# Kernel tuning notes

Hardware: AMD Instinct MI355X
Metric: run time of the kernel (lower is better)

The kernel has to match this reference:

```python
import jax, jax.numpy as jnp
import numpy as np

B, T, D = 32, 1024, 1024
PCA_DIM = 256
NS = 4
NC = 1024
SEC = PCA_DIM // NS


def setup_inputs() -> dict:
    key = jax.random.key(0)
    k1, k2, k3 = jax.random.split(key, 3)
    inputs = jax.random.normal(k1, (B, T, D), dtype=jnp.float32)
    # variance_scaling(1.0, 'fan_avg', 'normal'): std = sqrt(2 / (fan_in + fan_out))
    pca_proj = jax.random.normal(k2, (D, PCA_DIM), dtype=jnp.float32) * np.float32(np.sqrt(2.0 / (D + PCA_DIM)))
    pre_bias = jnp.zeros((1, D), dtype=jnp.float32)
    # per-section codebooks, variance_scaling(0.1, 'fan_avg', 'normal')
    codebooks = jax.random.normal(k3, (NS, NC, SEC), dtype=jnp.float32) * np.float32(np.sqrt(0.1 * 2.0 / (NC + SEC)))
    return {"inputs": inputs, "pca_proj": pca_proj, "pre_bias": pre_bias, "codebooks": codebooks}


def reference(inputs, pca_proj, pre_bias, codebooks):
    in_shape = inputs.shape
    d = in_shape[-1]
    flat = inputs.reshape(-1, d)  # [N, D]
    n = flat.shape[0]
    # --- PCA projection + reconstruction / decorrelation losses ---
    projected = (flat + pre_bias) @ pca_proj            # [N, P]
    unprojected = projected @ pca_proj.T - pre_bias     # [N, D]
    l2_loss = jnp.mean(jnp.sqrt(jnp.sum(jnp.square(flat - unprojected), axis=-1)))
    cov = projected.T @ projected / n                   # [P, P]
    cov_loss = jnp.mean(jnp.square(cov - jnp.eye(pca_proj.shape[1], dtype=projected.dtype)))
    pca_loss = l2_loss + cov_loss
    # --- per-section vector quantization ---
    ns, nc, sec = codebooks.shape
    secs = projected.reshape(n, ns, sec).transpose(1, 0, 2)  # [ns, N, sec] == jnp.split along -1

    def quantize_section(x, cb):
        # x: [N, sec], cb: [nc, sec]; squared-L2 cdist via expansion
        dist = (jnp.sum(x * x, axis=1, keepdims=True)
                - 2.0 * (x @ cb.T)
                + jnp.sum(cb * cb, axis=1)[None, :])    # [N, nc]
        idx = jnp.argmin(dist, axis=1)                  # [N]
        q = cb[idx]                                     # gather == one_hot @ cb
        loss = jnp.square(q - jax.lax.stop_gradient(x))  # [N, sec]
        q_st = x + jax.lax.stop_gradient(q - x)         # straight-through
        return q_st, loss, idx

    q, sec_loss, idx = jax.vmap(quantize_section)(secs, codebooks)  # [ns,N,sec] x2, [ns,N]
    quantized = q.transpose(1, 0, 2).reshape(n, ns * sec)           # concat sections -> [N, P]
    quantized = (quantized @ pca_proj.T - pre_bias).reshape(in_shape)  # pca_unproject
    nn_idx = idx.reshape((ns,) + in_shape[:-1])                     # [ns, B, T]
    quantization_loss = jnp.mean(sec_loss.reshape((ns,) + in_shape[:-1] + (sec,)), axis=0) + pca_loss
    codebook = jax.lax.stop_gradient(codebooks.reshape(ns * nc, sec))
    cluster_counts = jnp.ones((ns, nc), dtype=jnp.float32)  # eval mode: jnp.ones init, no EMA
    return quantized, quantization_loss, nn_idx, codebook, cluster_counts
```

## Files before the change

### kernel.cpp

```cpp
#include <hip/hip_runtime.h>
#include <math.h>

#define NROW 32768
#define DIM  1024
#define PDIM 256
#define NSEC 4
#define NCODE 1024
#define SECD 64

__global__ __launch_bounds__(256, 4) void k_proj(const float* __restrict__ X,
                                                 const float* __restrict__ W,
                                                 const float* __restrict__ bias,
                                                 float* __restrict__ p0) {
    __shared__ __align__(16) float As[16][68];
    __shared__ __align__(16) float Bs[16][256];
    const int t  = threadIdx.x;
    const int ry = t >> 5;
    const int rx = t & 31;
    const int rb = blockIdx.x * 64;
    const int z  = blockIdx.z;
    const int k0 = z * 384;
    const int kn = (z == 2) ? 256 : 384;
    const int lr = t >> 2;
    const int ks = (t & 3) * 4;
    const int wv = t >> 6;
    const int ln = t & 63;
    const int gsw = ((ln & 31) << 1) | (ln >> 5);
    float* outp = p0 + (size_t)z * ((size_t)NROW * PDIM);
    float acc[8][8] = {};
    for (int kc = k0; kc < k0 + kn; kc += 16) {
        #pragma unroll
        for (int j = 0; j < 4; ++j) {
            const int krow = wv * 4 + j;
            __builtin_amdgcn_global_load_lds(
                (const __attribute__((address_space(1))) void*)(W + (size_t)(kc + krow) * PDIM + gsw * 4),
                (__attribute__((address_space(3))) void*)(&Bs[krow][0]),
                16, 0, 0);
        }
        float4 a = *(const float4*)&X[(size_t)(rb + lr) * DIM + kc + ks];
        float4 c = *(const float4*)&bias[kc + ks];
        As[ks + 0][lr] = a.x + c.x;
        As[ks + 1][lr] = a.y + c.y;
        As[ks + 2][lr] = a.z + c.z;
        As[ks + 3][lr] = a.w + c.w;
        __syncthreads();
        #pragma unroll
        for (int k = 0; k < 16; ++k) {
            float4 x0 = *(const float4*)&As[k][ry * 8];
            float4 x1 = *(const float4*)&As[k][ry * 8 + 4];
            float4 y0 = *(const float4*)&Bs[k][rx * 4];
            float4 y1 = *(const float4*)&Bs[k][128 + rx * 4];
            float aa[8] = {x0.x, x0.y, x0.z, x0.w, x1.x, x1.y, x1.z, x1.w};
            float bb[8] = {y0.x, y0.y, y0.z, y0.w, y1.x, y1.y, y1.z, y1.w};
            #pragma unroll
            for (int i = 0; i < 8; ++i)
                #pragma unroll
                for (int j = 0; j < 8; ++j)
                    acc[i][j] = fmaf(aa[i], bb[j], acc[i][j]);
        }
        __syncthreads();
    }
    #pragma unroll
    for (int i = 0; i < 8; ++i) {
        const size_t base = (size_t)(rb + ry * 8 + i) * PDIM + rx * 8;
        *(float4*)&outp[base]     = make_float4(acc[i][0], acc[i][1], acc[i][2], acc[i][3]);
        *(float4*)&outp[base + 4] = make_float4(acc[i][4], acc[i][5], acc[i][6], acc[i][7]);
    }
}

__global__ __launch_bounds__(256) void k_comb(float* __restrict__ p) {
    const size_t i = ((size_t)blockIdx.x * 256 + threadIdx.x) * 4;
    float4 a = *(const float4*)&p[i];
    float4 b = *(const float4*)&p[i + 8388608];
    float4 c = *(const float4*)&p[i + 16777216];
    float4 r;
    r.x = __fadd_rn(__fadd_rn(a.x, b.x), c.x);
    r.y = __fadd_rn(__fadd_rn(a.y, b.y), c.y);
    r.z = __fadd_rn(__fadd_rn(a.z, b.z), c.z);
    r.w = __fadd_rn(__fadd_rn(a.w, b.w), c.w);
    *(float4*)&p[i] = r;
}

__global__ __launch_bounds__(256, 4) void k_pm(const float* __restrict__ P,
                                               const float* __restrict__ M,
                                               float* __restrict__ PMa,
                                               float* __restrict__ PMb) {
    __shared__ __align__(16) float As[16][68];
    __shared__ __align__(16) float Bs[16][256];
    const int t  = threadIdx.x;
    const int ry = t >> 5;
    const int rx = t & 31;
    const int rb = blockIdx.x * 64;
    const int z  = blockIdx.z;
    const int k0 = z * 128;
    const int lr = t >> 2;
    const int ks = (t & 3) * 4;
    const int wv = t >> 6;
    const int ln = t & 63;
    const int gsw = ((ln & 31) << 1) | (ln >> 5);
    float* outp = z ? PMb : PMa;
    float acc[8][8] = {};
    for (int kc = k0; kc < k0 + 128; kc += 16) {
        #pragma unroll
        for (int j = 0; j < 4; ++j) {
            const int krow = wv * 4 + j;
            __builtin_amdgcn_global_load_lds(
                (const __attribute__((address_space(1))) void*)(M + (size_t)(kc + krow) * PDIM + gsw * 4),
                (__attribute__((address_space(3))) void*)(&Bs[krow][0]),
                16, 0, 0);
        }
        float4 a = *(const float4*)&P[(size_t)(rb + lr) * PDIM + kc + ks];
        As[ks + 0][lr] = a.x;
        As[ks + 1][lr] = a.y;
        As[ks + 2][lr] = a.z;
        As[ks + 3][lr] = a.w;
        __syncthreads();
        #pragma unroll
        for (int k = 0; k < 16; ++k) {
            float4 x0 = *(const float4*)&As[k][ry * 8];
            float4 x1 = *(const float4*)&As[k][ry * 8 + 4];
            float4 y0 = *(const float4*)&Bs[k][rx * 4];
            float4 y1 = *(const float4*)&Bs[k][128 + rx * 4];
            float aa[8] = {x0.x, x0.y, x0.z, x0.w, x1.x, x1.y, x1.z, x1.w};
            float bb[8] = {y0.x, y0.y, y0.z, y0.w, y1.x, y1.y, y1.z, y1.w};
            #pragma unroll
            for (int i = 0; i < 8; ++i)
                #pragma unroll
                for (int j = 0; j < 8; ++j)
                    acc[i][j] = fmaf(aa[i], bb[j], acc[i][j]);
        }
        __syncthreads();
    }
    #pragma unroll
    for (int i = 0; i < 8; ++i) {
        const size_t base = (size_t)(rb + ry * 8 + i) * PDIM + rx * 8;
        *(float4*)&outp[base]     = make_float4(acc[i][0], acc[i][1], acc[i][2], acc[i][3]);
        *(float4*)&outp[base + 4] = make_float4(acc[i][4], acc[i][5], acc[i][6], acc[i][7]);
    }
}

__global__ __launch_bounds__(256) void k_wtw(const float* __restrict__ W,
                                             float* __restrict__ M) {
    __shared__ float As[16][64];
    __shared__ float Bs[16][64];
    const int t = threadIdx.x;
    const int tx = t & 15, ty = t >> 4;
    const int ib = blockIdx.x * 64;
    const int jb = blockIdx.y * 64;
    const int sk = t >> 4;
    const int sc = (t & 15) * 4;
    float acc[4][4] = {};
    for (int kc = 0; kc < DIM; kc += 16) {
        float4 a = *(const float4*)&W[(size_t)(kc + sk) * PDIM + ib + sc];
        float4 b = *(const float4*)&W[(size_t)(kc + sk) * PDIM + jb + sc];
        *(float4*)&As[sk][sc] = a;
        *(float4*)&Bs[sk][sc] = b;
        __syncthreads();
        #pragma unroll
        for (int k = 0; k < 16; ++k) {
            float4 a4 = *(const float4*)&As[k][ty * 4];
            float4 b4 = *(const float4*)&Bs[k][tx * 4];
            float aa[4] = {a4.x, a4.y, a4.z, a4.w};
            float bb[4] = {b4.x, b4.y, b4.z, b4.w};
            #pragma unroll
            for (int i = 0; i < 4; ++i)
                #pragma unroll
                for (int j = 0; j < 4; ++j)
                    acc[i][j] = fmaf(aa[i], bb[j], acc[i][j]);
        }
        __syncthreads();
    }
    #pragma unroll
    for (int i = 0; i < 4; ++i)
        #pragma unroll
        for (int j = 0; j < 4; ++j)
            M[(size_t)(ib + ty * 4 + i) * PDIM + jb + tx * 4 + j] = acc[i][j];
}

__global__ __launch_bounds__(256) void k_xn2(const float* __restrict__ X,
                                             const float* __restrict__ bias,
                                             float* __restrict__ xn2) {
    const int n = blockIdx.x * 4 + (threadIdx.x >> 6);
    const int lane = threadIdx.x & 63;
    float s = 0.0f;
    #pragma unroll
    for (int i = 0; i < 4; ++i) {
        float4 x = *(const float4*)&X[(size_t)n * DIM + i * 256 + lane * 4];
        float4 b = *(const float4*)&bias[i * 256 + lane * 4];
        float vx = x.x + b.x, vy = x.y + b.y, vz = x.z + b.z, vw = x.w + b.w;
        s = fmaf(vx, vx, s); s = fmaf(vy, vy, s);
        s = fmaf(vz, vz, s); s = fmaf(vw, vw, s);
    }
    #pragma unroll
    for (int o = 1; o < 64; o <<= 1) s += __shfl_xor(s, o);
    if (lane == 0) xn2[n] = s;
}

__global__ __launch_bounds__(256) void k_rowres(const float* __restrict__ P,
                                                const float* __restrict__ PMa,
                                                const float* __restrict__ PMb,
                                                const float* __restrict__ xn2,
                                                float* __restrict__ rowres) {
    const int n = blockIdx.x * 4 + (threadIdx.x >> 6);
    const int lane = threadIdx.x & 63;
    float4 p  = *(const float4*)&P[(size_t)n * PDIM + lane * 4];
    float4 pa = *(const float4*)&PMa[(size_t)n * PDIM + lane * 4];
    float4 pb = *(const float4*)&PMb[(size_t)n * PDIM + lane * 4];
    float s = 0.0f;
    s = fmaf(p.x, (pa.x + pb.x) - 2.0f * p.x, s);
    s = fmaf(p.y, (pa.y + pb.y) - 2.0f * p.y, s);
    s = fmaf(p.z, (pa.z + pb.z) - 2.0f * p.z, s);
    s = fmaf(p.w, (pa.w + pb.w) - 2.0f * p.w, s);
    #pragma unroll
    for (int o = 1; o < 64; o <<= 1) s += __shfl_xor(s, o);
    if (lane == 0) rowres[n] = xn2[n] + s;
}

__global__ __launch_bounds__(256) void k_cov(const float* __restrict__ Pm,
                                             float* __restrict__ cov) {
    __shared__ float As[16][64];
    __shared__ float Bs[16][64];
    const int t = threadIdx.x;
    const int tx = t & 15, ty = t >> 4;
    const int ib = blockIdx.x * 64;
    const int jb = blockIdx.y * 64;
    const int nb = blockIdx.z * 2048;
    const int sk = t >> 4;
    const int sc = (t & 15) * 4;
    float acc[4][4] = {};
    for (int kc = 0; kc < 2048; kc += 16) {
        float4 a = *(const float4*)&Pm[(size_t)(nb + kc + sk) * PDIM + ib + sc];
        float4 b = *(const float4*)&Pm[(size_t)(nb + kc + sk) * PDIM + jb + sc];
        *(float4*)&As[sk][sc] = a;
        *(float4*)&Bs[sk][sc] = b;
        __syncthreads();
        #pragma unroll
        for (int k = 0; k < 16; ++k) {
            float4 a4 = *(const float4*)&As[k][ty * 4];
            float4 b4 = *(const float4*)&Bs[k][tx * 4];
            float aa[4] = {a4.x, a4.y, a4.z, a4.w};
            float bb[4] = {b4.x, b4.y, b4.z, b4.w};
            #pragma unroll
            for (int i = 0; i < 4; ++i)
                #pragma unroll
                for (int j = 0; j < 4; ++j)
                    acc[i][j] = fmaf(aa[i], bb[j], acc[i][j]);
        }
        __syncthreads();
    }
    #pragma unroll
    for (int i = 0; i < 4; ++i)
        #pragma unroll
        for (int j = 0; j < 4; ++j)
            atomicAdd(&cov[(size_t)(ib + ty * 4 + i) * PDIM + jb + tx * 4 + j], acc[i][j]);
}

__global__ __launch_bounds__(256) void k_covloss(const float* __restrict__ cov,
                                                 float* __restrict__ scal) {
    const int t = threadIdx.x;
    float s = 0.0f;
    for (int e = t; e < PDIM * PDIM; e += 256) {
        int i = e >> 8, j = e & 255;
        float v = cov[e] * (1.0f / 32768.0f) - (i == j ? 1.0f : 0.0f);
        s = fmaf(v, v, s);
    }
    #pragma unroll
    for (int o = 1; o < 64; o <<= 1) s += __shfl_xor(s, o);
    __shared__ float r4[4];
    if ((t & 63) == 0) r4[t >> 6] = s;
    __syncthreads();
    if (t == 0) scal[1] = (r4[0] + r4[1] + r4[2] + r4[3]) * (1.0f / 65536.0f);
}

__global__ __launch_bounds__(256) void k_l2(const float* __restrict__ rowres,
                                            float* __restrict__ scal) {
    int r = blockIdx.x * 256 + threadIdx.x;
    float v = sqrtf(rowres[r]);
    #pragma unroll
    for (int o = 1; o < 64; o <<= 1) v += __shfl_xor(v, o);
    if ((threadIdx.x & 63) == 0) atomicAdd(&scal[0], v);
}

__global__ __launch_bounds__(256) void k_cnorm(const float* __restrict__ cbs,
                                               float* __restrict__ cnorm) {
    int c = blockIdx.x * 256 + threadIdx.x;
    const float* p = &cbs[(size_t)c * SECD];
    float a[8];
    #pragma unroll
    for (int j = 0; j < 8; ++j) a[j] = __fmul_rn(p[j], p[j]);
    #pragma unroll
    for (int i = 8; i < 64; i += 8)
        #pragma unroll
        for (int j = 0; j < 8; ++j)
            a[j] = __fadd_rn(a[j], __fmul_rn(p[i + j], p[i + j]));
    float r = __fadd_rn(__fadd_rn(__fadd_rn(a[0], a[1]), __fadd_rn(a[2], a[3])),
                        __fadd_rn(__fadd_rn(a[4], a[5]), __fadd_rn(a[6], a[7])));
    cnorm[c] = r;
}

__global__ __launch_bounds__(256) void k_vq(const float* __restrict__ proj,
                                            const float* __restrict__ cbs,
                                            const float* __restrict__ cnorm,
                                            int* __restrict__ widx,
                                            float* __restrict__ out_idx,
                                            float* __restrict__ out_qloss) {
    __shared__ float xs[64][64];
    __shared__ float cs[64][128];
    __shared__ float xnorm[64];
    __shared__ int   sidx[64];
    const int t = threadIdx.x;
    const int ry = t >> 5;
    const int tx = t & 31;
    const int rb = blockIdx.x * 64;
    const int lr = t >> 2;
    const int kq = (t & 3) * 16;
    const int cr = t >> 1;
    const int ko = (t & 1) * 32;
    float qacc[16];
    #pragma unroll
    for (int i = 0; i < 16; ++i) qacc[i] = 0.0f;

    for (int s = 0; s < NSEC; ++s) {
        #pragma unroll
        for (int i = 0; i < 16; i += 4) {
            float4 v = *(const float4*)&proj[(size_t)(rb + lr) * PDIM + s * SECD + kq + i];
            xs[kq + i + 0][lr] = v.x; xs[kq + i + 1][lr] = v.y;
            xs[kq + i + 2][lr] = v.z; xs[kq + i + 3][lr] = v.w;
        }
        __syncthreads();
        if (t < 64) {
            float a[8];
            #pragma unroll
            for (int j = 0; j < 8; ++j) { float v = xs[j][t]; a[j] = __fmul_rn(v, v); }
            #pragma unroll
            for (int i = 8; i < 64; i += 8)
                #pragma unroll
                for (int j = 0; j < 8; ++j) {
                    float v = xs[i + j][t];
                    a[j] = __fadd_rn(a[j], __fmul_rn(v, v));
                }
            xnorm[t] = __fadd_rn(__fadd_rn(__fadd_rn(a[0], a[1]), __fadd_rn(a[2], a[3])),
                                 __fadd_rn(__fadd_rn(a[4], a[5]), __fadd_rn(a[6], a[7])));
        }
        float best[8]; int bidx[8];
        #pragma unroll
        for (int i = 0; i < 8; ++i) { best[i] = 3.4e38f; bidx[i] = 0; }

        for (int ct = 0; ct < 8; ++ct) {
            __syncthreads();
            #pragma unroll
            for (int u = 0; u < 32; u += 4) {
                float4 v = *(const float4*)&cbs[(size_t)(s * NCODE + ct * 128 + cr) * SECD + ko + u];
                cs[ko + u + 0][cr] = v.x; cs[ko + u + 1][cr] = v.y;
                cs[ko + u + 2][cr] = v.z; cs[ko + u + 3][cr] = v.w;
            }
            __syncthreads();
            float4 cn4 = *(const float4*)&cnorm[s * NCODE + ct * 128 + tx * 4];
            float cna[4] = {cn4.x, cn4.y, cn4.z, cn4.w};
            float acc[8][4] = {};
            #pragma unroll 8
            for (int k = 0; k < 64; ++k) {
                float4 x0 = *(const float4*)&xs[k][ry * 8];
                float4 x1 = *(const float4*)&xs[k][ry * 8 + 4];
                float4 b4 = *(const float4*)&cs[k][tx * 4];
                float aa[8] = {x0.x, x0.y, x0.z, x0.w, x1.x, x1.y, x1.z, x1.w};
                float bb[4] = {b4.x, b4.y, b4.z, b4.w};
                #pragma unroll
                for (int i = 0; i < 8; ++i)
                    #pragma unroll
                    for (int j = 0; j < 4; ++j)
                        acc[i][j] = fmaf(aa[i], bb[j], acc[i][j]);
            }
            #pragma unroll
            for (int i = 0; i < 8; ++i) {
                float xn = xnorm[ry * 8 + i];
                #pragma unroll
                for (int j = 0; j < 4; ++j) {
                    float d = __fadd_rn(__fsub_rn(xn, __fmul_rn(2.0f, acc[i][j])), cna[j]);
                    int code = ct * 128 + tx * 4 + j;
                    if (d < best[i]) { best[i] = d; bidx[i] = code; }
                }
            }
        }
        #pragma unroll
        for (int i = 0; i < 8; ++i) {
            float d = best[i]; int ix = bidx[i];
            #pragma unroll
            for (int o = 1; o < 32; o <<= 1) {
                float od = __shfl_xor(d, o);
                int   oi = __shfl_xor(ix, o);
                if (od < d || (od == d && oi < ix)) { d = od; ix = oi; }
            }
            if (tx == 0) {
                int row = rb + ry * 8 + i;
                widx[s * NROW + row] = ix;
                out_idx[s * NROW + row] = (float)ix;
                sidx[ry * 8 + i] = ix;
            }
        }
        __syncthreads();
        {
            const float* crow = &cbs[(size_t)(s * NCODE + sidx[lr]) * SECD];
            #pragma unroll
            for (int i = 0; i < 16; i += 4) {
                float4 q = *(const float4*)&crow[kq + i];
                float qq[4] = {q.x, q.y, q.z, q.w};
                #pragma unroll
                for (int u = 0; u < 4; ++u) {
                    float d = qq[u] - xs[kq + i + u][lr];
                    qacc[i + u] = fmaf(d, d, qacc[i + u]);
                }
            }
        }
        __syncthreads();
    }
    #pragma unroll
    for (int i = 0; i < 16; i += 4) {
        float4 v = make_float4(0.25f * qacc[i + 0], 0.25f * qacc[i + 1],
                               0.25f * qacc[i + 2], 0.25f * qacc[i + 3]);
        *(float4*)&out_qloss[(size_t)(rb + lr) * SECD + kq + i] = v;
    }
}

__global__ __launch_bounds__(256) void k_cbu(const float* __restrict__ cbs,
                                             const float* __restrict__ W,
                                             float* __restrict__ cbu) {
    __shared__ float As[16][64];
    __shared__ float Bs[16][64];
    const int t = threadIdx.x;
    const int tx = t & 15, ty = t >> 4;
    const int s = blockIdx.z;
    const int cbase = blockIdx.y * 64;
    const int db = blockIdx.x * 64;
    const int lr = t >> 2;
    const int lk = (t & 3) * 4;
    float acc[4][4] = {};
    for (int kc = 0; kc < SECD; kc += 16) {
        float4 a = *(const float4*)&cbs[(size_t)(s * NCODE + cbase + lr) * SECD + kc + lk];
        float4 b = *(const float4*)&W[(size_t)(db + lr) * PDIM + s * SECD + kc + lk];
        As[lk + 0][lr] = a.x; As[lk + 1][lr] = a.y;
        As[lk + 2][lr] = a.z; As[lk + 3][lr] = a.w;
        Bs[lk + 0][lr] = b.x; Bs[lk + 1][lr] = b.y;
        Bs[lk + 2][lr] = b.z; Bs[lk + 3][lr] = b.w;
        __syncthreads();
        #pragma unroll
        for (int k = 0; k < 16; ++k) {
            float4 a4 = *(const float4*)&As[k][ty * 4];
            float4 b4 = *(const float4*)&Bs[k][tx * 4];
            float aa[4] = {a4.x, a4.y, a4.z, a4.w};
            float bb[4] = {b4.x, b4.y, b4.z, b4.w};
            #pragma unroll
            for (int i = 0; i < 4; ++i)
                #pragma unroll
                for (int j = 0; j < 4; ++j)
                    acc[i][j] = fmaf(aa[i], bb[j], acc[i][j]);
        }
        __syncthreads();
    }
    #pragma unroll
    for (int i = 0; i < 4; ++i) {
        float4 v = make_float4(acc[i][0], acc[i][1], acc[i][2], acc[i][3]);
        *(float4*)&cbu[(size_t)(s * NCODE + cbase + ty * 4 + i) * DIM + db + tx * 4] = v;
    }
}

__global__ __launch_bounds__(256) void k_gather(const float* __restrict__ cbu,
                                                const int* __restrict__ widx,
                                                const float* __restrict__ bias,
                                                float* __restrict__ out0) {
    const int n = blockIdx.x;
    const int d = threadIdx.x * 4;
    int i0 = widx[0 * NROW + n];
    int i1 = widx[1 * NROW + n];
    int i2 = widx[2 * NROW + n];
    int i3 = widx[3 * NROW + n];
    float4 v0 = *(const float4*)&cbu[((size_t)(0 * NCODE + i0)) * DIM + d];
    float4 v1 = *(const float4*)&cbu[((size_t)(1 * NCODE + i1)) * DIM + d];
    float4 v2 = *(const float4*)&cbu[((size_t)(2 * NCODE + i2)) * DIM + d];
    float4 v3 = *(const float4*)&cbu[((size_t)(3 * NCODE + i3)) * DIM + d];
    float4 b = *(const float4*)&bias[d];
    float4 r;
    r.x = v0.x + v1.x + v2.x + v3.x - b.x;
    r.y = v0.y + v1.y + v2.y + v3.y - b.y;
    r.z = v0.z + v1.z + v2.z + v3.z - b.z;
    r.w = v0.w + v1.w + v2.w + v3.w - b.w;
    *(float4*)&out0[(size_t)n * DIM + d] = r;
}

__global__ __launch_bounds__(256) void k_addpca(float* __restrict__ out1,
                                                const float* __restrict__ scal) {
    float pca = scal[0] * (1.0f / 32768.0f) + scal[1];
    int e = blockIdx.x * 256 + threadIdx.x;
    float4* p = (float4*)out1;
    float4 v = p[e];
    v.x += pca; v.y += pca; v.z += pca; v.w += pca;
    p[e] = v;
}

__global__ __launch_bounds__(256) void k_tail(const float* __restrict__ cbs,
                                              float* __restrict__ out3,
                                              float* __restrict__ out4) {
    int e = blockIdx.x * 256 + threadIdx.x;
    ((float4*)out3)[e] = ((const float4*)cbs)[e];
    if (e < 4096) out4[e] = 1.0f;
}

extern "C" void kernel_launch(void* const* d_in, const int* in_sizes, int n_in,
                              void* d_out, int out_size, void* d_ws, size_t ws_size,
                              hipStream_t stream) {
    (void)in_sizes; (void)n_in; (void)out_size; (void)ws_size;
    const float* X    = (const float*)d_in[0];
    const float* W    = (const float*)d_in[1];
    const float* bias = (const float*)d_in[2];
    const float* cbs  = (const float*)d_in[3];

    float* out  = (float*)d_out;
    float* out0 = out;
    float* out1 = out + 33554432;
    float* out2 = out + 35651584;
    float* out3 = out + 35782656;
    float* out4 = out + 36044800;

    char* ws = (char*)d_ws;
    float* cbu    = (float*)(ws);
    float* rowres = (float*)(ws + 16777216);
    float* cov    = (float*)(ws + 16908288);
    float* scal   = (float*)(ws + 17170432);
    float* cnorm  = (float*)(ws + 17170496);
    int*   widx   = (int*)  (ws + 17186880);
    float* wtw    = (float*)(ws + 17711168);

    float* proj = out0;
    float* PMa  = out0 + 8388608;
    float* PMb  = out0 + 25165824;
    float* xn2  = out1;

    hipMemsetAsync(ws + 16908288, 0, 262144 + 64, stream);

    k_proj    <<<dim3(512, 1, 3), 256, 0, stream>>>(X, W, bias, proj);
    k_comb    <<<8192,            256, 0, stream>>>(proj);
    k_xn2     <<<8192,            256, 0, stream>>>(X, bias, xn2);
    k_wtw     <<<dim3(4, 4),      256, 0, stream>>>(W, wtw);
    k_cov     <<<dim3(4, 4, 16),  256, 0, stream>>>(proj, cov);
    k_covloss <<<1,               256, 0, stream>>>(cov, scal);
    k_pm      <<<dim3(512, 1, 2), 256, 0, stream>>>(proj, wtw, PMa, PMb);
    k_rowres  <<<8192,            256, 0, stream>>>(proj, PMa, PMb, xn2, rowres);
    k_l2      <<<128,             256, 0, stream>>>(rowres, scal);
    k_cnorm   <<<16,              256, 0, stream>>>(cbs, cnorm);
    k_vq      <<<512,             256, 0, stream>>>(proj, cbs, cnorm, widx, out2, out1);
    k_cbu     <<<dim3(16, 16, 4), 256, 0, stream>>>(cbs, W, cbu);
    k_gather  <<<32768,           256, 0, stream>>>(cbu, widx, bias, out0);
    k_addpca  <<<2048,            256, 0, stream>>>(out1, scal);
    k_tail    <<<256,             256, 0, stream>>>(cbs, out3, out4);
}
```

Before: 1.084 ms.

## Parallelize VQ over sections via grid dim and split cov reduction finer

New measurement: 1.057 ms. 2.5% less time.

```diff
diff --git a/kernel.cpp b/kernel.cpp
--- a/kernel.cpp
+++ b/kernel.cpp
@@ -224,11 +224,11 @@
     const int tx = t & 15, ty = t >> 4;
     const int ib = blockIdx.x * 64;
     const int jb = blockIdx.y * 64;
-    const int nb = blockIdx.z * 2048;
+    const int nb = blockIdx.z * 512;
     const int sk = t >> 4;
     const int sc = (t & 15) * 4;
     float acc[4][4] = {};
-    for (int kc = 0; kc < 2048; kc += 16) {
+    for (int kc = 0; kc < 512; kc += 16) {
         float4 a = *(const float4*)&Pm[(size_t)(nb + kc + sk) * PDIM + ib + sc];
         float4 b = *(const float4*)&Pm[(size_t)(nb + kc + sk) * PDIM + jb + sc];
         *(float4*)&As[sk][sc] = a;
@@ -303,7 +303,7 @@
                                             const float* __restrict__ cnorm,
                                             int* __restrict__ widx,
                                             float* __restrict__ out_idx,
-                                            float* __restrict__ out_qloss) {
+                                            float* __restrict__ qpart) {
     __shared__ float xs[64][64];
     __shared__ float cs[64][128];
     __shared__ float xnorm[64];
@@ -312,113 +312,105 @@
     const int ry = t >> 5;
     const int tx = t & 31;
     const int rb = blockIdx.x * 64;
+    const int s  = blockIdx.y;
     const int lr = t >> 2;
     const int kq = (t & 3) * 16;
     const int cr = t >> 1;
     const int ko = (t & 1) * 32;
-    float qacc[16];
-    #pragma unroll
-    for (int i = 0; i < 16; ++i) qacc[i] = 0.0f;
-
-    for (int s = 0; s < NSEC; ++s) {
+
+    #pragma unroll
+    for (int i = 0; i < 16; i += 4) {
+        float4 v = *(const float4*)&proj[(size_t)(rb + lr) * PDIM + s * SECD + kq + i];
+        xs[kq + i + 0][lr] = v.x; xs[kq + i + 1][lr] = v.y;
+        xs[kq + i + 2][lr] = v.z; xs[kq + i + 3][lr] = v.w;
+    }
+    __syncthreads();
+    if (t < 64) {
+        float a[8];
+        #pragma unroll
+        for (int j = 0; j < 8; ++j) { float v = xs[j][t]; a[j] = __fmul_rn(v, v); }
+        #pragma unroll
+        for (int i = 8; i < 64; i += 8)
+            #pragma unroll
+            for (int j = 0; j < 8; ++j) {
+                float v = xs[i + j][t];
+                a[j] = __fadd_rn(a[j], __fmul_rn(v, v));
+            }
+        xnorm[t] = __fadd_rn(__fadd_rn(__fadd_rn(a[0], a[1]), __fadd_rn(a[2], a[3])),
+                             __fadd_rn(__fadd_rn(a[4], a[5]), __fadd_rn(a[6], a[7])));
+    }
+    float best[8]; int bidx[8];
+    #pragma unroll
+    for (int i = 0; i < 8; ++i) { best[i] = 3.4e38f; bidx[i] = 0; }
+
+    for (int ct = 0; ct < 8; ++ct) {
+        __syncthreads();
+        #pragma unroll
+        for (int u = 0; u < 32; u += 4) {
+            float4 v = *(const float4*)&cbs[(size_t)(s * NCODE + ct * 128 + cr) * SECD + ko + u];
+            cs[ko + u + 0][cr] = v.x; cs[ko + u + 1][cr] = v.y;
+            cs[ko + u + 2][cr] = v.z; cs[ko + u + 3][cr] = v.w;
+        }
+        __syncthreads();
+        float4 cn4 = *(const float4*)&cnorm[s * NCODE + ct * 128 + tx * 4];
+        float cna[4] = {cn4.x, cn4.y, cn4.z, cn4.w};
+        float acc[8][4] = {};
+        #pragma unroll 8
+        for (int k = 0; k < 64; ++k) {
+            float4 x0 = *(const float4*)&xs[k][ry * 8];
+            float4 x1 = *(const float4*)&xs[k][ry * 8 + 4];
+            float4 b4 = *(const float4*)&cs[k][tx * 4];
+            float aa[8] = {x0.x, x0.y, x0.z, x0.w, x1.x, x1.y, x1.z, x1.w};
+            float bb[4] = {b4.x, b4.y, b4.z, b4.w};
+            #pragma unroll
+            for (int i = 0; i < 8; ++i)
+                #pragma unroll
+                for (int j = 0; j < 4; ++j)
+                    acc[i][j] = fmaf(aa[i], bb[j], acc[i][j]);
+        }
+        #pragma unroll
+        for (int i = 0; i < 8; ++i) {
+            float xn = xnorm[ry * 8 + i];
+            #pragma unroll
+            for (int j = 0; j < 4; ++j) {
+                float d = __fadd_rn(__fsub_rn(xn, __fmul_rn(2.0f, acc[i][j])), cna[j]);
+                int code = ct * 128 + tx * 4 + j;
+                if (d < best[i]) { best[i] = d; bidx[i] = code; }
+            }
+        }
+    }
+    #pragma unroll
+    for (int i = 0; i < 8; ++i) {
+        float d = best[i]; int ix = bidx[i];
+        #pragma unroll
+        for (int o = 1; o < 32; o <<= 1) {
+            float od = __shfl_xor(d, o);
+            int   oi = __shfl_xor(ix, o);
+            if (od < d || (od == d && oi < ix)) { d = od; ix = oi; }
+        }
+        if (tx == 0) {
+            int row = rb + ry * 8 + i;
+            widx[s * NROW + row] = ix;
+            out_idx[s * NROW + row] = (float)ix;
+            sidx[ry * 8 + i] = ix;
+        }
+    }
+    __syncthreads();
+    {
+        const float* crow = &cbs[(size_t)(s * NCODE + sidx[lr]) * SECD];
         #pragma unroll
         for (int i = 0; i < 16; i += 4) {
-            float4 v = *(const float4*)&proj[(size_t)(rb + lr) * PDIM + s * SECD + kq + i];
-            xs[kq + i + 0][lr] = v.x; xs[kq + i + 1][lr] = v.y;
-            xs[kq + i + 2][lr] = v.z; xs[kq + i + 3][lr] = v.w;
-        }
-        __syncthreads();
-        if (t < 64) {
-            float a[8];
-            #pragma unroll
-            for (int j = 0; j < 8; ++j) { float v = xs[j][t]; a[j] = __fmul_rn(v, v); }
-            #pragma unroll
-            for (int i = 8; i < 64; i += 8)
-                #pragma unroll
-                for (int j = 0; j < 8; ++j) {
-                    float v = xs[i + j][t];
-                    a[j] = __fadd_rn(a[j], __fmul_rn(v, v));
-                }
-            xnorm[t] = __fadd_rn(__fadd_rn(__fadd_rn(a[0], a[1]), __fadd_rn(a[2], a[3])),
-                                 __fadd_rn(__fadd_rn(a[4], a[5]), __fadd_rn(a[6], a[7])));
-        }
-        float best[8]; int bidx[8];
-        #pragma unroll
-        for (int i = 0; i < 8; ++i) { best[i] = 3.4e38f; bidx[i] = 0; }
-
-        for (int ct = 0; ct < 8; ++ct) {
-            __syncthreads();
-            #pragma unroll
-            for (int u = 0; u < 32; u += 4) {
-                float4 v = *(const float4*)&cbs[(size_t)(s * NCODE + ct * 128 + cr) * SECD + ko + u];
-                cs[ko + u + 0][cr] = v.x; cs[ko + u + 1][cr] = v.y;
-                cs[ko + u + 2][cr] = v.z; cs[ko + u + 3][cr] = v.w;
+            float4 q = *(const float4*)&crow[kq + i];
+            float qq[4] = {q.x, q.y, q.z, q.w};
+            float r[4];
+            #pragma unroll
+            for (int u = 0; u < 4; ++u) {
+                float d = qq[u] - xs[kq + i + u][lr];
+                r[u] = __fmul_rn(d, d);
             }
-            __syncthreads();
-            float4 cn4 = *(const float4*)&cnorm[s * NCODE + ct * 128 + tx * 4];
-            float cna[4] = {cn4.x, cn4.y, cn4.z, cn4.w};
-            float acc[8][4] = {};
-            #pragma unroll 8
-            for (int k = 0; k < 64; ++k) {
-                float4 x0 = *(const float4*)&xs[k][ry * 8];
-                float4 x1 = *(const float4*)&xs[k][ry * 8 + 4];
-                float4 b4 = *(const float4*)&cs[k][tx * 4];
-                float aa[8] = {x0.x, x0.y, x0.z, x0.w, x1.x, x1.y, x1.z, x1.w};
-                float bb[4] = {b4.x, b4.y, b4.z, b4.w};
-                #pragma unroll
-                for (int i = 0; i < 8; ++i)
-                    #pragma unroll
-                    for (int j = 0; j < 4; ++j)
-                        acc[i][j] = fmaf(aa[i], bb[j], acc[i][j]);
-            }
-            #pragma unroll
-            for (int i = 0; i < 8; ++i) {
-                float xn = xnorm[ry * 8 + i];
-                #pragma unroll
-                for (int j = 0; j < 4; ++j) {
-                    float d = __fadd_rn(__fsub_rn(xn, __fmul_rn(2.0f, acc[i][j])), cna[j]);
-                    int code = ct * 128 + tx * 4 + j;
-                    if (d < best[i]) { best[i] = d; bidx[i] = code; }
-                }
-            }
-        }
-        #pragma unroll
-        for (int i = 0; i < 8; ++i) {
-            float d = best[i]; int ix = bidx[i];
-            #pragma unroll
-            for (int o = 1; o < 32; o <<= 1) {
-                float od = __shfl_xor(d, o);
-                int   oi = __shfl_xor(ix, o);
-                if (od < d || (od == d && oi < ix)) { d = od; ix = oi; }
-            }
-            if (tx == 0) {
-                int row = rb + ry * 8 + i;
-                widx[s * NROW + row] = ix;
-                out_idx[s * NROW + row] = (float)ix;
-                sidx[ry * 8 + i] = ix;
-            }
-        }
-        __syncthreads();
-        {
-            const float* crow = &cbs[(size_t)(s * NCODE + sidx[lr]) * SECD];
-            #pragma unroll
-            for (int i = 0; i < 16; i += 4) {
-                float4 q = *(const float4*)&crow[kq + i];
-                float qq[4] = {q.x, q.y, q.z, q.w};
-                #pragma unroll
-                for (int u = 0; u < 4; ++u) {
-                    float d = qq[u] - xs[kq + i + u][lr];
-                    qacc[i + u] = fmaf(d, d, qacc[i + u]);
-                }
-            }
-        }
-        __syncthreads();
-    }
-    #pragma unroll
-    for (int i = 0; i < 16; i += 4) {
-        float4 v = make_float4(0.25f * qacc[i + 0], 0.25f * qacc[i + 1],
-                               0.25f * qacc[i + 2], 0.25f * qacc[i + 3]);
-        *(float4*)&out_qloss[(size_t)(rb + lr) * SECD + kq + i] = v;
+            *(float4*)&qpart[((size_t)s * NROW + rb + lr) * SECD + kq + i] =
+                make_float4(r[0], r[1], r[2], r[3]);
+        }
     }
 }
 
@@ -488,13 +480,20 @@
 }
 
 __global__ __launch_bounds__(256) void k_addpca(float* __restrict__ out1,
+                                                const float* __restrict__ qpart,
                                                 const float* __restrict__ scal) {
     float pca = scal[0] * (1.0f / 32768.0f) + scal[1];
-    int e = blockIdx.x * 256 + threadIdx.x;
-    float4* p = (float4*)out1;
-    float4 v = p[e];
-    v.x += pca; v.y += pca; v.z += pca; v.w += pca;
-    p[e] = v;
+    const size_t e = ((size_t)blockIdx.x * 256 + threadIdx.x) * 4;
+    float4 a = *(const float4*)&qpart[e];
+    float4 b = *(const float4*)&qpart[e + 2097152];
+    float4 c = *(const float4*)&qpart[e + 4194304];
+    float4 d = *(const float4*)&qpart[e + 6291456];
+    float4 r;
+    r.x = 0.25f * __fadd_rn(__fadd_rn(__fadd_rn(a.x, b.x), c.x), d.x) + pca;
+    r.y = 0.25f * __fadd_rn(__fadd_rn(__fadd_rn(a.y, b.y), c.y), d.y) + pca;
+    r.z = 0.25f * __fadd_rn(__fadd_rn(__fadd_rn(a.z, b.z), c.z), d.z) + pca;
+    r.w = 0.25f * __fadd_rn(__fadd_rn(__fadd_rn(a.w, b.w), c.w), d.w) + pca;
+    *(float4*)&out1[e] = r;
 }
 
 __global__ __launch_bounds__(256) void k_tail(const float* __restrict__ cbs,
@@ -530,9 +529,10 @@
     int*   widx   = (int*)  (ws + 17186880);
     float* wtw    = (float*)(ws + 17711168);
 
-    float* proj = out0;
-    float* PMa  = out0 + 8388608;
-    float* PMb  = out0 + 25165824;
+    float* proj  = out0;
+    float* PMa   = out0 + 8388608;
+    float* PMb   = out0 + 25165824;
+    float* qpart = out0 + 8388608;
     float* xn2  = out1;
 
     hipMemsetAsync(ws + 16908288, 0, 262144 + 64, stream);
@@ -541,15 +541,15 @@
     k_comb    <<<8192,            256, 0, stream>>>(proj);
     k_xn2     <<<8192,            256, 0, stream>>>(X, bias, xn2);
     k_wtw     <<<dim3(4, 4),      256, 0, stream>>>(W, wtw);
-    k_cov     <<<dim3(4, 4, 16),  256, 0, stream>>>(proj, cov);
+    k_cov     <<<dim3(4, 4, 64),  256, 0, stream>>>(proj, cov);
     k_covloss <<<1,               256, 0, stream>>>(cov, scal);
     k_pm      <<<dim3(512, 1, 2), 256, 0, stream>>>(proj, wtw, PMa, PMb);
     k_rowres  <<<8192,            256, 0, stream>>>(proj, PMa, PMb, xn2, rowres);
     k_l2      <<<128,             256, 0, stream>>>(rowres, scal);
     k_cnorm   <<<16,              256, 0, stream>>>(cbs, cnorm);
-    k_vq      <<<512,             256, 0, stream>>>(proj, cbs, cnorm, widx, out2, out1);
+    k_vq      <<<dim3(512, 4),    256, 0, stream>>>(proj, cbs, cnorm, widx, out2, qpart);
     k_cbu     <<<dim3(16, 16, 4), 256, 0, stream>>>(cbs, W, cbu);
     k_gather  <<<32768,           256, 0, stream>>>(cbu, widx, bias, out0);
-    k_addpca  <<<2048,            256, 0, stream>>>(out1, scal);
+    k_addpca  <<<2048,            256, 0, stream>>>(out1, qpart, scal);
     k_tail    <<<256,             256, 0, stream>>>(cbs, out3, out4);
 }
```
